# Performance work log

Hardware: AMD Instinct MI355X
Metric: run time of the kernel (lower is better)

## Reference

```python
import jax
import jax.numpy as jnp
from jax import lax
import numpy as np

BETA = 0.5
IPOT_ITERS = 50
IPOT_K = 1
EPS = 1e-5  # F.normalize eps


def _l2_normalize(x, eps=EPS):
    n = jnp.linalg.norm(x, axis=-1, keepdims=True)
    return x / jnp.maximum(n, eps)


def cost_matrix_cosine(x, y):
    # x: [b, m, d], y: [b, n, d] -> 1 - cosine_sim : [b, m, n]
    return 1.0 - jnp.einsum('bmd,bnd->bmn', _l2_normalize(x), _l2_normalize(y))


def ipot(C, x_len, x_pad, y_len, y_pad, joint_pad, beta, iteration, k):
    # C: [b, m, n] (txt x img). Mirrors UNITER's ipot (no_grad).
    b, m, n = C.shape
    jp_T = jnp.swapaxes(joint_pad, 1, 2)                      # [b, n, m]
    A = jnp.where(jp_T, 0.0, jnp.exp(-jnp.swapaxes(C, 1, 2) / beta))  # [b, n, m]
    T0 = jnp.where(jp_T, 0.0, jnp.ones((b, n, m), C.dtype))
    sigma0 = jnp.where(x_pad, 0.0, 1.0 / x_len[:, None])      # [b, m]
    xl = x_len[:, None, None]
    yl = y_len[:, None, None]
    x_mask = (x_pad.astype(C.dtype) * 1e4)[:, None, :]        # [b, 1, m]
    y_mask = (y_pad.astype(C.dtype) * 1e4)[:, None, :]        # [b, 1, n]

    def outer(carry, _):
        T, sigma = carry
        Q = A * T                                             # [b, n, m]
        def inner(sig, _):
            # sig: [b, m]
            qs = jnp.einsum('bnm,bm->bn', Q, sig)[:, None, :]  # [b, 1, n]
            delta = 1.0 / (yl * qs + y_mask)                   # [b, 1, n]
            sig_new = 1.0 / (xl * jnp.matmul(delta, Q) + x_mask)  # [b, 1, m]
            return sig_new[:, 0, :], delta
        sigma, deltas = lax.scan(inner, sigma, None, length=k)
        delta = deltas[-1]                                     # [b, 1, n]
        T = delta[:, 0, :, None] * Q * sigma[:, None, :]       # [b, n, m]
        return (T, sigma), None

    (T, _), _ = lax.scan(outer, (T0, sigma0), None, length=iteration)
    return jnp.where(jp_T, 0.0, T)


def optimal_transport_dist(txt_emb, img_emb, txt_pad, img_pad,
                           beta=BETA, iteration=IPOT_ITERS, k=IPOT_K):
    cost = cost_matrix_cosine(txt_emb, img_emb)               # [b, tl, il]
    joint_pad = txt_pad[:, :, None] | img_pad[:, None, :]
    cost = jnp.where(joint_pad, 0.0, cost)
    txt_len = (txt_pad.shape[1] - jnp.sum(txt_pad, axis=1)).astype(cost.dtype)
    img_len = (img_pad.shape[1] - jnp.sum(img_pad, axis=1)).astype(cost.dtype)
    T = ipot(lax.stop_gradient(cost), txt_len, txt_pad, img_len, img_pad,
             joint_pad, beta, iteration, k)                   # [b, il, tl]
    T = lax.stop_gradient(T)
    # trace(cost @ T) without materializing [b, tl, tl]
    return jnp.einsum('bmn,bnm->b', cost, T)


def setup_inputs() -> dict:
    key = jax.random.key(0)
    ks = jax.random.split(key, 6)
    B, TL, IL, D = 256, 128, 100, 768
    sequence_output = jax.random.normal(ks[0], (B, TL + IL, D), dtype=jnp.float32)
    input_ids = jax.random.randint(ks[1], (B, TL), 0, 30522)
    image_feat = jax.random.normal(ks[2], (B, IL, D), dtype=jnp.float32)
    # realistic padding: valid prefix of random length, padded suffix
    txt_len = jax.random.randint(ks[3], (B,), TL // 2, TL + 1)
    img_len = jax.random.randint(ks[4], (B,), IL // 2, IL + 1)
    txt_pad = jnp.arange(TL)[None, :] >= txt_len[:, None]
    img_pad = jnp.arange(IL)[None, :] >= img_len[:, None]
    is_correct = jax.random.randint(ks[5], (B,), 0, 2)
    return {
        'sequence_output': sequence_output,
        'input_ids': input_ids,
        'image_feat': image_feat,
        'txt_pad': txt_pad,
        'img_pad': img_pad,
        'is_correct': is_correct,
    }


def reference(sequence_output, input_ids, image_feat, txt_pad, img_pad, is_correct):
    tl = input_ids.shape[1]
    il = image_feat.shape[1]
    txt_emb = sequence_output[:, :tl, :].astype(jnp.float32)
    img_emb = sequence_output[:, tl:tl + il, :].astype(jnp.float32)
    ot_dist = optimal_transport_dist(txt_emb, img_emb, txt_pad, img_pad)
    ot_dist = ot_dist.astype(sequence_output.dtype)
    pos = is_correct == 1
    neg = is_correct == 0
    pos_sum = jnp.sum(jnp.where(pos, ot_dist, 0.0))
    neg_sum = jnp.sum(jnp.where(neg, ot_dist, 0.0))
    denom = jnp.sum(pos) + jnp.sum(neg)
    ot_loss = (pos_sum - neg_sum) / denom.astype(ot_dist.dtype)
    return ot_loss


if __name__ == '__main__':
    out = reference(**setup_inputs())
    print(out)
```

## Files before the change

### kernel.cpp

```cpp
#include <hip/hip_runtime.h>
#include <math.h>
#include <stdint.h>

#define TL 128
#define IL 100
#define NP 112
#define DIM 768
#define NSEQ 228
#define KT 32
#define NT 256
#define ITERS 50
#define XROW 72

typedef float f32x4 __attribute__((ext_vector_type(4)));
typedef short short8 __attribute__((ext_vector_type(8)));

__device__ __forceinline__ uint16_t f2bf(float x) {
    union { float f; uint32_t u; } v; v.f = x;
    uint32_t r = v.u + 0x7FFFu + ((v.u >> 16) & 1u);
    return (uint16_t)(r >> 16);
}
__device__ __forceinline__ float bf2f(uint16_t h) {
    union { float f; uint32_t u; } v; v.u = ((uint32_t)h) << 16;
    return v.f;
}

__global__ void __launch_bounds__(NT, 1)
WRA_ot_kernel(const float* __restrict__ seq,
              const int* __restrict__ txt_pad,
              const int* __restrict__ img_pad,
              const int* __restrict__ is_correct,
              float* __restrict__ out, int nblocks)
{
    __shared__ __align__(16) union {
        struct {
            uint16_t X[TL * XROW];
            uint16_t Y[NP * XROW];
        } g;
        float As[224 * 64];
    } u;
    __shared__ __align__(16) float sums[NSEQ];
    __shared__ __align__(16) float xm[TL];
    __shared__ __align__(16) float ym[NP];
    __shared__ __align__(16) float inx[TL];
    __shared__ __align__(16) float iny[NP];
    __shared__ __align__(16) float wp[2][4][TL];
    __shared__ float red[4];
    __shared__ int cnt[2];

    const int t    = threadIdx.x;
    const int b    = blockIdx.x;
    const int w    = t >> 6;
    const int lane = t & 63;

    if (t < 2) cnt[t] = 0;
    if (t < NSEQ) sums[t] = 0.0f;
    __syncthreads();
    if (t < TL) {
        int p = txt_pad[b * TL + t] ? 1 : 0;
        xm[t] = p ? 1e4f : 0.0f;
        if (p) atomicAdd(&cnt[0], 1);
    } else if (t < TL + IL) {
        int p = img_pad[b * IL + (t - TL)] ? 1 : 0;
        ym[t - TL] = p ? 1e4f : 0.0f;
        if (p) atomicAdd(&cnt[1], 1);
    } else if (t < TL + NP) {
        ym[t - TL] = 1e4f;
    }

    const float* Xg = seq + (size_t)b * NSEQ * DIM;
    const float* Yg = Xg + (size_t)TL * DIM;

    const float* gp[8];
    uint16_t*    dp[8];
    int   srow[8];
    bool  act[8];
    float nrm[8];
    float4 v[8];
#pragma unroll
    for (int r = 0; r < 8; r++) {
        int f = t + NT * r;
        act[r] = (f < 1824);
        nrm[r] = 0.0f;
        int f2 = act[r] ? f : 0;
        bool isX = (f2 < 1024);
        int row = isX ? (f2 >> 3) : ((f2 - 1024) >> 3);
        int kc  = (f2 & 7) << 2;
        gp[r] = (isX ? Xg : Yg) + row * DIM + kc;
        int nq  = ((kc >> 3) + row) & 3;
        dp[r] = (isX ? u.g.X : u.g.Y) + row * XROW + nq * 8 + (kc & 7);
        srow[r] = isX ? row : (TL + row);
    }
    {
        uint32_t* y32 = (uint32_t*)u.g.Y;
        for (int i = IL * (XROW/2) + t; i < NP * (XROW/2); i += NT) y32[i] = 0;
    }
#pragma unroll
    for (int r = 0; r < 8; r++) if (act[r]) v[r] = *(const float4*)(gp[r]);

    f32x4 acc[2][7];
#pragma unroll
    for (int a = 0; a < 2; a++)
#pragma unroll
        for (int q = 0; q < 7; q++) acc[a][q] = (f32x4){0.f, 0.f, 0.f, 0.f};

    const int lr = lane & 15, lq = lane >> 4;
    for (int c = 0; c < 24; c++) {
        __syncthreads();
#pragma unroll
        for (int r = 0; r < 8; r++) if (act[r]) {
            float4 x = v[r];
            nrm[r] += x.x*x.x + x.y*x.y + x.z*x.z + x.w*x.w;
            uint16_t h0 = f2bf(x.x), h1 = f2bf(x.y), h2 = f2bf(x.z), h3 = f2bf(x.w);
            uint16_t l0 = f2bf(x.x - bf2f(h0)), l1 = f2bf(x.y - bf2f(h1));
            uint16_t l2 = f2bf(x.z - bf2f(h2)), l3 = f2bf(x.w - bf2f(h3));
            uint64_t hq  = (uint64_t)h0 | ((uint64_t)h1<<16) | ((uint64_t)h2<<32) | ((uint64_t)h3<<48);
            uint64_t lq8 = (uint64_t)l0 | ((uint64_t)l1<<16) | ((uint64_t)l2<<32) | ((uint64_t)l3<<48);
            *(uint64_t*)(dp[r])      = hq;
            *(uint64_t*)(dp[r] + 32) = lq8;
            if (c < 23) v[r] = *(const float4*)(gp[r] + (c + 1) * KT);
        }
        __syncthreads();
        short8 ah[2], al[2], bh[7], bl[7];
#pragma unroll
        for (int a = 0; a < 2; a++) {
            int m = 16 * (2*w + a) + lr;
            int base = m * XROW + 8 * ((lq + m) & 3);
            ah[a] = *(const short8*)&u.g.X[base];
            al[a] = *(const short8*)&u.g.X[base + 32];
        }
#pragma unroll
        for (int q = 0; q < 7; q++) {
            int n = 16 * q + lr;
            int base = n * XROW + 8 * ((lq + n) & 3);
            bh[q] = *(const short8*)&u.g.Y[base];
            bl[q] = *(const short8*)&u.g.Y[base + 32];
        }
#pragma unroll
        for (int a = 0; a < 2; a++)
#pragma unroll
            for (int q = 0; q < 7; q++) {
                acc[a][q] = __builtin_amdgcn_mfma_f32_16x16x32_bf16(ah[a], bh[q], acc[a][q], 0, 0, 0);
                acc[a][q] = __builtin_amdgcn_mfma_f32_16x16x32_bf16(ah[a], bl[q], acc[a][q], 0, 0, 0);
                acc[a][q] = __builtin_amdgcn_mfma_f32_16x16x32_bf16(al[a], bh[q], acc[a][q], 0, 0, 0);
            }
    }

    __syncthreads();
#pragma unroll
    for (int r = 0; r < 8; r++) if (act[r]) atomicAdd(&sums[srow[r]], nrm[r]);
#pragma unroll
    for (int a = 0; a < 2; a++)
#pragma unroll
        for (int q = 0; q < 7; q++)
#pragma unroll
            for (int rg = 0; rg < 4; rg++) {
                int m = 16 * (2*w + a) + 4*lq + rg;
                int n = 16 * q + lr;
                int tp = (m >> 3) + ((n >> 3) << 4);
                u.As[(tp << 6) + ((n & 7) << 3) + (m & 7)] = acc[a][q][rg];
            }
    __syncthreads();
    if (t < TL)            inx[t]      = 1.0f / fmaxf(sqrtf(sums[t]), 1e-5f);
    else if (t < NSEQ)     iny[t - TL] = 1.0f / fmaxf(sqrtf(sums[t]), 1e-5f);
    else if (t < TL + NP)  iny[t - TL] = 1.0f;
    __syncthreads();

    const float xlen = (float)(TL - cnt[0]);
    const float ylen = (float)(IL - cnt[1]);
    const int mI = t & 15, nI = t >> 4;

    float rx[8], xmv[8], ry[8], ymv[8];
    {
        float4 a0 = *(const float4*)&inx[8*mI], a1 = *(const float4*)&inx[8*mI + 4];
        rx[0]=a0.x; rx[1]=a0.y; rx[2]=a0.z; rx[3]=a0.w;
        rx[4]=a1.x; rx[5]=a1.y; rx[6]=a1.z; rx[7]=a1.w;
        float4 b0 = *(const float4*)&xm[8*mI], b1 = *(const float4*)&xm[8*mI + 4];
        xmv[0]=b0.x; xmv[1]=b0.y; xmv[2]=b0.z; xmv[3]=b0.w;
        xmv[4]=b1.x; xmv[5]=b1.y; xmv[6]=b1.z; xmv[7]=b1.w;
        if (nI < 14) {
            float4 c0 = *(const float4*)&iny[8*nI], c1 = *(const float4*)&iny[8*nI + 4];
            ry[0]=c0.x; ry[1]=c0.y; ry[2]=c0.z; ry[3]=c0.w;
            ry[4]=c1.x; ry[5]=c1.y; ry[6]=c1.z; ry[7]=c1.w;
            float4 d0 = *(const float4*)&ym[8*nI], d1 = *(const float4*)&ym[8*nI + 4];
            ymv[0]=d0.x; ymv[1]=d0.y; ymv[2]=d0.z; ymv[3]=d0.w;
            ymv[4]=d1.x; ymv[5]=d1.y; ymv[6]=d1.z; ymv[7]=d1.w;
        } else {
#pragma unroll
            for (int j = 0; j < 8; j++) { ry[j] = 1.0f; ymv[j] = 1e4f; }
        }
    }

    float aa[8][8], qq[8][8];
    if (nI < 14) {
#pragma unroll
        for (int j = 0; j < 8; j++) {
            float4 d0 = *(const float4*)&u.As[(t << 6) + (j << 3)];
            float4 d1 = *(const float4*)&u.As[(t << 6) + (j << 3) + 4];
            float dv[8] = {d0.x, d0.y, d0.z, d0.w, d1.x, d1.y, d1.z, d1.w};
#pragma unroll
            for (int i = 0; i < 8; i++) {
                bool pad = (xmv[i] > 0.0f) || (ymv[j] > 0.0f);
                float cc = pad ? 0.0f : (1.0f - dv[i] * rx[i] * ry[j]);
                float av = pad ? 0.0f : expf(-2.0f * cc);
                aa[j][i] = av; qq[j][i] = av;
            }
        }
    } else {
#pragma unroll
        for (int j = 0; j < 8; j++)
#pragma unroll
            for (int i = 0; i < 8; i++) { aa[j][i] = 0.0f; qq[j][i] = 0.0f; }
    }

    float sg[8];
#pragma unroll
    for (int i = 0; i < 8; i++) sg[i] = (xmv[i] > 0.0f) ? 0.0f : (1.0f / xlen);

    float dl[8];
    for (int it = 0; it < ITERS; ++it) {
        float p[8];
#pragma unroll
        for (int j = 0; j < 8; j++)
            p[j] = qq[j][0]*sg[0] + qq[j][1]*sg[1] + qq[j][2]*sg[2] + qq[j][3]*sg[3]
                 + qq[j][4]*sg[4] + qq[j][5]*sg[5] + qq[j][6]*sg[6] + qq[j][7]*sg[7];
#pragma unroll
        for (int j = 0; j < 8; j++) {
            p[j] += __shfl_xor(p[j], 1);
            p[j] += __shfl_xor(p[j], 2);
            p[j] += __shfl_xor(p[j], 4);
            p[j] += __shfl_xor(p[j], 8);
            dl[j] = __builtin_amdgcn_rcpf(ylen * p[j] + ymv[j]);
        }
        float sp[8];
#pragma unroll
        for (int i = 0; i < 8; i++) {
            float s = dl[0]*qq[0][i] + dl[1]*qq[1][i] + dl[2]*qq[2][i] + dl[3]*qq[3][i]
                    + dl[4]*qq[4][i] + dl[5]*qq[5][i] + dl[6]*qq[6][i] + dl[7]*qq[7][i];
            s += __shfl_xor(s, 16);
            s += __shfl_xor(s, 32);
            sp[i] = s;
        }
        if (lane < 16) {
            float* wrow = &wp[it & 1][w][8 * mI];
            *(float4*)wrow       = make_float4(sp[0], sp[1], sp[2], sp[3]);
            *(float4*)(wrow + 4) = make_float4(sp[4], sp[5], sp[6], sp[7]);
        }
        __syncthreads();
#pragma unroll
        for (int i = 0; i < 8; i += 4) {
            float4 s0 = *(const float4*)&wp[it & 1][0][8*mI + i];
            float4 s1 = *(const float4*)&wp[it & 1][1][8*mI + i];
            float4 s2 = *(const float4*)&wp[it & 1][2][8*mI + i];
            float4 s3 = *(const float4*)&wp[it & 1][3][8*mI + i];
            sg[i+0] = __builtin_amdgcn_rcpf(xlen*(s0.x+s1.x+s2.x+s3.x) + xmv[i+0]);
            sg[i+1] = __builtin_amdgcn_rcpf(xlen*(s0.y+s1.y+s2.y+s3.y) + xmv[i+1]);
            sg[i+2] = __builtin_amdgcn_rcpf(xlen*(s0.z+s1.z+s2.z+s3.z) + xmv[i+2]);
            sg[i+3] = __builtin_amdgcn_rcpf(xlen*(s0.w+s1.w+s2.w+s3.w) + xmv[i+3]);
        }
        if (it < ITERS - 1) {
#pragma unroll
            for (int j = 0; j < 8; j++) {
                float dj = dl[j];
#pragma unroll
                for (int i = 0; i < 8; i++)
                    qq[j][i] = (qq[j][i] * aa[j][i]) * (dj * sg[i]);
            }
        }
    }

    float local = 0.0f;
#pragma unroll
    for (int j = 0; j < 8; j++)
#pragma unroll
        for (int i = 0; i < 8; i++) {
            float av = aa[j][i];
            float cc = (av > 0.0f) ? (-0.5f * logf(av)) : 0.0f;
            local += cc * qq[j][i] * (dl[j] * sg[i]);
        }
    local += __shfl_xor(local, 1);
    local += __shfl_xor(local, 2);
    local += __shfl_xor(local, 4);
    local += __shfl_xor(local, 8);
    local += __shfl_xor(local, 16);
    local += __shfl_xor(local, 32);
    if (lane == 0) red[w] = local;
    __syncthreads();
    if (t == 0) {
        float tot = red[0] + red[1] + red[2] + red[3];
        float sgn = (is_correct[b] == 1) ? 1.0f : -1.0f;
        atomicAdd(out, sgn * tot / (float)nblocks);
    }
}

extern "C" void kernel_launch(void* const* d_in, const int* in_sizes, int n_in,
                              void* d_out, int out_size, void* d_ws, size_t ws_size,
                              hipStream_t stream) {
    const float* seq   = (const float*)d_in[0];
    const int* txt_pad = (const int*)d_in[3];
    const int* img_pad = (const int*)d_in[4];
    const int* is_corr = (const int*)d_in[5];
    float* out = (float*)d_out;
    const int B = in_sizes[5];

    hipMemsetAsync(out, 0, sizeof(float), stream);
    WRA_ot_kernel<<<B, NT, 0, stream>>>(seq, txt_pad, img_pad, is_corr, out, B);
}
```

Baseline: 374.2 us.

## Double threads per block to 512 and re-tile GEMM and IPOT iteration

Raises the block size from 256 to 512 threads (8 waves) and splits the cosine GEMM across a 4x2 wave grid, with each wave computing up to 4 N-tiles instead of 7. The IPOT iteration state per thread is halved to 8x4 and now lives in a new XOR-swizzled shared-memory layout, with the cross-wave partial-sum buffer folded into the shared union. The goal is more parallelism and lower register pressure per thread during the serial 50-iteration loop. In exchange, each iteration's cross-wave reduction gets longer (7 partial rows instead of 4), and the barrier now synchronises twice as many waves.

```diff
diff --git a/kernel.cpp b/kernel.cpp
--- a/kernel.cpp
+++ b/kernel.cpp
@@ -8,7 +8,8 @@
 #define DIM 768
 #define NSEQ 228
 #define KT 32
-#define NT 256
+#define NT 512
+#define NWAVE 8
 #define ITERS 50
 #define XROW 72
 
@@ -25,7 +26,16 @@
     return v.f;
 }
 
-__global__ void __launch_bounds__(NT, 1)
+__device__ __forceinline__ float xorsum32(float x) {
+    x += __shfl_xor(x, 1);
+    x += __shfl_xor(x, 2);
+    x += __shfl_xor(x, 4);
+    x += __shfl_xor(x, 8);
+    x += __shfl_xor(x, 16);
+    return x;
+}
+
+__global__ void __launch_bounds__(NT, 2)
 WRA_ot_kernel(const float* __restrict__ seq,
               const int* __restrict__ txt_pad,
               const int* __restrict__ img_pad,
@@ -37,15 +47,15 @@
             uint16_t X[TL * XROW];
             uint16_t Y[NP * XROW];
         } g;
-        float As[224 * 64];
+        float As[448 * 32];
+        float wp[2][7][TL];
     } u;
     __shared__ __align__(16) float sums[NSEQ];
     __shared__ __align__(16) float xm[TL];
     __shared__ __align__(16) float ym[NP];
     __shared__ __align__(16) float inx[TL];
     __shared__ __align__(16) float iny[NP];
-    __shared__ __align__(16) float wp[2][4][TL];
-    __shared__ float red[4];
+    __shared__ float red[NWAVE];
     __shared__ int cnt[2];
 
     const int t    = threadIdx.x;
@@ -71,14 +81,14 @@
     const float* Xg = seq + (size_t)b * NSEQ * DIM;
     const float* Yg = Xg + (size_t)TL * DIM;
 
-    const float* gp[8];
-    uint16_t*    dp[8];
-    int   srow[8];
-    bool  act[8];
-    float nrm[8];
-    float4 v[8];
-#pragma unroll
-    for (int r = 0; r < 8; r++) {
+    const float* gp[4];
+    uint16_t*    dp[4];
+    int   srow[4];
+    bool  act[4];
+    float nrm[4];
+    float4 v[4];
+#pragma unroll
+    for (int r = 0; r < 4; r++) {
         int f = t + NT * r;
         act[r] = (f < 1824);
         nrm[r] = 0.0f;
@@ -96,19 +106,22 @@
         for (int i = IL * (XROW/2) + t; i < NP * (XROW/2); i += NT) y32[i] = 0;
     }
 #pragma unroll
-    for (int r = 0; r < 8; r++) if (act[r]) v[r] = *(const float4*)(gp[r]);
-
-    f32x4 acc[2][7];
+    for (int r = 0; r < 4; r++) if (act[r]) v[r] = *(const float4*)(gp[r]);
+
+    const int wm = w >> 1;
+    const int wn = w & 1;
+    const int NQ = wn ? 3 : 4;
+    f32x4 acc[2][4];
 #pragma unroll
     for (int a = 0; a < 2; a++)
 #pragma unroll
-        for (int q = 0; q < 7; q++) acc[a][q] = (f32x4){0.f, 0.f, 0.f, 0.f};
+        for (int q = 0; q < 4; q++) acc[a][q] = (f32x4){0.f, 0.f, 0.f, 0.f};
 
     const int lr = lane & 15, lq = lane >> 4;
     for (int c = 0; c < 24; c++) {
         __syncthreads();
 #pragma unroll
-        for (int r = 0; r < 8; r++) if (act[r]) {
+        for (int r = 0; r < 4; r++) if (act[r]) {
             float4 x = v[r];
             nrm[r] += x.x*x.x + x.y*x.y + x.z*x.z + x.w*x.w;
             uint16_t h0 = f2bf(x.x), h1 = f2bf(x.y), h2 = f2bf(x.z), h3 = f2bf(x.w);
@@ -121,17 +134,17 @@
             if (c < 23) v[r] = *(const float4*)(gp[r] + (c + 1) * KT);
         }
         __syncthreads();
-        short8 ah[2], al[2], bh[7], bl[7];
+        short8 ah[2], al[2], bh[4], bl[4];
 #pragma unroll
         for (int a = 0; a < 2; a++) {
-            int m = 16 * (2*w + a) + lr;
+            int m = 16 * (2*wm + a) + lr;
             int base = m * XROW + 8 * ((lq + m) & 3);
             ah[a] = *(const short8*)&u.g.X[base];
             al[a] = *(const short8*)&u.g.X[base + 32];
         }
 #pragma unroll
-        for (int q = 0; q < 7; q++) {
-            int n = 16 * q + lr;
+        for (int q = 0; q < 4; q++) if (q < NQ) {
+            int n = 16 * (4*wn + q) + lr;
             int base = n * XROW + 8 * ((lq + n) & 3);
             bh[q] = *(const short8*)&u.g.Y[base];
             bl[q] = *(const short8*)&u.g.Y[base + 32];
@@ -139,7 +152,7 @@
 #pragma unroll
         for (int a = 0; a < 2; a++)
 #pragma unroll
-            for (int q = 0; q < 7; q++) {
+            for (int q = 0; q < 4; q++) if (q < NQ) {
                 acc[a][q] = __builtin_amdgcn_mfma_f32_16x16x32_bf16(ah[a], bh[q], acc[a][q], 0, 0, 0);
                 acc[a][q] = __builtin_amdgcn_mfma_f32_16x16x32_bf16(ah[a], bl[q], acc[a][q], 0, 0, 0);
                 acc[a][q] = __builtin_amdgcn_mfma_f32_16x16x32_bf16(al[a], bh[q], acc[a][q], 0, 0, 0);
@@ -148,17 +161,18 @@
 
     __syncthreads();
 #pragma unroll
-    for (int r = 0; r < 8; r++) if (act[r]) atomicAdd(&sums[srow[r]], nrm[r]);
+    for (int r = 0; r < 4; r++) if (act[r]) atomicAdd(&sums[srow[r]], nrm[r]);
 #pragma unroll
     for (int a = 0; a < 2; a++)
 #pragma unroll
-        for (int q = 0; q < 7; q++)
+        for (int q = 0; q < 4; q++) if (q < NQ)
 #pragma unroll
             for (int rg = 0; rg < 4; rg++) {
-                int m = 16 * (2*w + a) + 4*lq + rg;
-                int n = 16 * q + lr;
-                int tp = (m >> 3) + ((n >> 3) << 4);
-                u.As[(tp << 6) + ((n & 7) << 3) + (m & 7)] = acc[a][q][rg];
+                int m = 16 * (2*wm + a) + 4*lq + rg;
+                int n = 16 * (4*wn + q) + lr;
+                int tp = (m >> 2) + ((n >> 3) << 5);
+                int cell = (((n & 7) ^ (tp & 7)) << 2) + (m & 3);
+                u.As[(tp << 5) + cell] = acc[a][q][rg];
             }
     __syncthreads();
     if (t < TL)            inx[t]      = 1.0f / fmaxf(sqrtf(sums[t]), 1e-5f);
@@ -168,17 +182,17 @@
 
     const float xlen = (float)(TL - cnt[0]);
     const float ylen = (float)(IL - cnt[1]);
-    const int mI = t & 15, nI = t >> 4;
-
-    float rx[8], xmv[8], ry[8], ymv[8];
+    const int mI = lane & 31;
+    const int nI = t >> 5;
+    const bool activeN = (nI < 14);
+
+    float rx[4], xmv[4], ry[8], ymv[8];
     {
-        float4 a0 = *(const float4*)&inx[8*mI], a1 = *(const float4*)&inx[8*mI + 4];
+        float4 a0 = *(const float4*)&inx[4*mI];
         rx[0]=a0.x; rx[1]=a0.y; rx[2]=a0.z; rx[3]=a0.w;
-        rx[4]=a1.x; rx[5]=a1.y; rx[6]=a1.z; rx[7]=a1.w;
-        float4 b0 = *(const float4*)&xm[8*mI], b1 = *(const float4*)&xm[8*mI + 4];
+        float4 b0 = *(const float4*)&xm[4*mI];
         xmv[0]=b0.x; xmv[1]=b0.y; xmv[2]=b0.z; xmv[3]=b0.w;
-        xmv[4]=b1.x; xmv[5]=b1.y; xmv[6]=b1.z; xmv[7]=b1.w;
-        if (nI < 14) {
+        if (activeN) {
             float4 c0 = *(const float4*)&iny[8*nI], c1 = *(const float4*)&iny[8*nI + 4];
             ry[0]=c0.x; ry[1]=c0.y; ry[2]=c0.z; ry[3]=c0.w;
             ry[4]=c1.x; ry[5]=c1.y; ry[6]=c1.z; ry[7]=c1.w;
@@ -191,15 +205,14 @@
         }
     }
 
-    float aa[8][8], qq[8][8];
-    if (nI < 14) {
+    float aa[8][4], qq[8][4];
+    if (activeN) {
 #pragma unroll
         for (int j = 0; j < 8; j++) {
-            float4 d0 = *(const float4*)&u.As[(t << 6) + (j << 3)];
-            float4 d1 = *(const float4*)&u.As[(t << 6) + (j << 3) + 4];
-            float dv[8] = {d0.x, d0.y, d0.z, d0.w, d1.x, d1.y, d1.z, d1.w};
-#pragma unroll
-            for (int i = 0; i < 8; i++) {
+            float4 d0 = *(const float4*)&u.As[(t << 5) + ((j ^ (t & 7)) << 2)];
+            float dv[4] = {d0.x, d0.y, d0.z, d0.w};
+#pragma unroll
+            for (int i = 0; i < 4; i++) {
                 bool pad = (xmv[i] > 0.0f) || (ymv[j] > 0.0f);
                 float cc = pad ? 0.0f : (1.0f - dv[i] * rx[i] * ry[j]);
                 float av = pad ? 0.0f : expf(-2.0f * cc);
@@ -210,60 +223,56 @@
 #pragma unroll
         for (int j = 0; j < 8; j++)
 #pragma unroll
-            for (int i = 0; i < 8; i++) { aa[j][i] = 0.0f; qq[j][i] = 0.0f; }
-    }
-
-    float sg[8];
-#pragma unroll
-    for (int i = 0; i < 8; i++) sg[i] = (xmv[i] > 0.0f) ? 0.0f : (1.0f / xlen);
+            for (int i = 0; i < 4; i++) { aa[j][i] = 0.0f; qq[j][i] = 0.0f; }
+    }
+    __syncthreads();
+
+    float sg[4];
+#pragma unroll
+    for (int i = 0; i < 4; i++) sg[i] = (xmv[i] > 0.0f) ? 0.0f : (1.0f / xlen);
 
     float dl[8];
     for (int it = 0; it < ITERS; ++it) {
-        float p[8];
-#pragma unroll
-        for (int j = 0; j < 8; j++)
-            p[j] = qq[j][0]*sg[0] + qq[j][1]*sg[1] + qq[j][2]*sg[2] + qq[j][3]*sg[3]
-                 + qq[j][4]*sg[4] + qq[j][5]*sg[5] + qq[j][6]*sg[6] + qq[j][7]*sg[7];
 #pragma unroll
         for (int j = 0; j < 8; j++) {
-            p[j] += __shfl_xor(p[j], 1);
-            p[j] += __shfl_xor(p[j], 2);
-            p[j] += __shfl_xor(p[j], 4);
-            p[j] += __shfl_xor(p[j], 8);
-            dl[j] = __builtin_amdgcn_rcpf(ylen * p[j] + ymv[j]);
-        }
-        float sp[8];
-#pragma unroll
-        for (int i = 0; i < 8; i++) {
+            float pj = qq[j][0]*sg[0] + qq[j][1]*sg[1] + qq[j][2]*sg[2] + qq[j][3]*sg[3];
+            pj = xorsum32(pj);
+            dl[j] = __builtin_amdgcn_rcpf(ylen * pj + ymv[j]);
+        }
+        float sp[4];
+#pragma unroll
+        for (int i = 0; i < 4; i++) {
             float s = dl[0]*qq[0][i] + dl[1]*qq[1][i] + dl[2]*qq[2][i] + dl[3]*qq[3][i]
                     + dl[4]*qq[4][i] + dl[5]*qq[5][i] + dl[6]*qq[6][i] + dl[7]*qq[7][i];
-            s += __shfl_xor(s, 16);
-            s += __shfl_xor(s, 32);
-            sp[i] = s;
-        }
-        if (lane < 16) {
-            float* wrow = &wp[it & 1][w][8 * mI];
-            *(float4*)wrow       = make_float4(sp[0], sp[1], sp[2], sp[3]);
-            *(float4*)(wrow + 4) = make_float4(sp[4], sp[5], sp[6], sp[7]);
+            sp[i] = s + __shfl_xor(s, 32);
+        }
+        if (w < 7 && lane < 32) {
+            *(float4*)&u.wp[it & 1][w][4 * mI] = make_float4(sp[0], sp[1], sp[2], sp[3]);
         }
         __syncthreads();
-#pragma unroll
-        for (int i = 0; i < 8; i += 4) {
-            float4 s0 = *(const float4*)&wp[it & 1][0][8*mI + i];
-            float4 s1 = *(const float4*)&wp[it & 1][1][8*mI + i];
-            float4 s2 = *(const float4*)&wp[it & 1][2][8*mI + i];
-            float4 s3 = *(const float4*)&wp[it & 1][3][8*mI + i];
-            sg[i+0] = __builtin_amdgcn_rcpf(xlen*(s0.x+s1.x+s2.x+s3.x) + xmv[i+0]);
-            sg[i+1] = __builtin_amdgcn_rcpf(xlen*(s0.y+s1.y+s2.y+s3.y) + xmv[i+1]);
-            sg[i+2] = __builtin_amdgcn_rcpf(xlen*(s0.z+s1.z+s2.z+s3.z) + xmv[i+2]);
-            sg[i+3] = __builtin_amdgcn_rcpf(xlen*(s0.w+s1.w+s2.w+s3.w) + xmv[i+3]);
+        {
+            float4 s0 = *(const float4*)&u.wp[it & 1][0][4*mI];
+            float4 s1 = *(const float4*)&u.wp[it & 1][1][4*mI];
+            float4 s2 = *(const float4*)&u.wp[it & 1][2][4*mI];
+            float4 s3 = *(const float4*)&u.wp[it & 1][3][4*mI];
+            float4 s4 = *(const float4*)&u.wp[it & 1][4][4*mI];
+            float4 s5 = *(const float4*)&u.wp[it & 1][5][4*mI];
+            float4 s6 = *(const float4*)&u.wp[it & 1][6][4*mI];
+            float t0 = s0.x+s1.x+s2.x+s3.x+s4.x+s5.x+s6.x;
+            float t1 = s0.y+s1.y+s2.y+s3.y+s4.y+s5.y+s6.y;
+            float t2 = s0.z+s1.z+s2.z+s3.z+s4.z+s5.z+s6.z;
+            float t3 = s0.w+s1.w+s2.w+s3.w+s4.w+s5.w+s6.w;
+            sg[0] = __builtin_amdgcn_rcpf(xlen*t0 + xmv[0]);
+            sg[1] = __builtin_amdgcn_rcpf(xlen*t1 + xmv[1]);
+            sg[2] = __builtin_amdgcn_rcpf(xlen*t2 + xmv[2]);
+            sg[3] = __builtin_amdgcn_rcpf(xlen*t3 + xmv[3]);
         }
         if (it < ITERS - 1) {
 #pragma unroll
             for (int j = 0; j < 8; j++) {
                 float dj = dl[j];
 #pragma unroll
-                for (int i = 0; i < 8; i++)
+                for (int i = 0; i < 4; i++)
                     qq[j][i] = (qq[j][i] * aa[j][i]) * (dj * sg[i]);
             }
         }
@@ -273,21 +282,17 @@
 #pragma unroll
     for (int j = 0; j < 8; j++)
 #pragma unroll
-        for (int i = 0; i < 8; i++) {
+        for (int i = 0; i < 4; i++) {
             float av = aa[j][i];
             float cc = (av > 0.0f) ? (-0.5f * logf(av)) : 0.0f;
             local += cc * qq[j][i] * (dl[j] * sg[i]);
         }
-    local += __shfl_xor(local, 1);
-    local += __shfl_xor(local, 2);
-    local += __shfl_xor(local, 4);
-    local += __shfl_xor(local, 8);
-    local += __shfl_xor(local, 16);
+    local = xorsum32(local);
     local += __shfl_xor(local, 32);
     if (lane == 0) red[w] = local;
     __syncthreads();
     if (t == 0) {
-        float tot = red[0] + red[1] + red[2] + red[3];
+        float tot = red[0] + red[1] + red[2] + red[3] + red[4] + red[5] + red[6] + red[7];
         float sgn = (is_correct[b] == 1) ? 1.0f : -1.0f;
         atomicAdd(out, sgn * tot / (float)nblocks);
     }
```

New measurement: 377.0 us. About the same (+0.7%).
